# Performance work log

Measured on AMD Instinct MI355X. Metric: run time of the kernel, lower is better.

Reference implementation:

```python
import jax, jax.numpy as jnp
import numpy as np

S = 256  # vocab_size == num_states (required for the original code to broadcast)
B = 16
L = 512


def sparsemax(z):
    # sparsemax over the last axis (Martins & Astudillo 2016)
    zs = -jnp.sort(-z, axis=-1)                      # descending sort
    k = jnp.arange(1, z.shape[-1] + 1, dtype=z.dtype)
    zc = jnp.cumsum(zs, axis=-1)
    supp = 1.0 + k * zs > zc                         # support mask
    kz = supp.sum(axis=-1, keepdims=True)
    tau = (jnp.take_along_axis(zc, kz - 1, axis=-1) - 1.0) / kz.astype(z.dtype)
    return jnp.maximum(z - tau, 0.0)


def sparsemax_loss_vec(z):
    # Fenchel-Young sparsemax loss against EVERY class y:
    #   loss[..., y] = <z, p*> - 0.5||p*||^2 + 0.5 - z_y,  p* = sparsemax(z)
    p = sparsemax(z)
    c = (z * p).sum(-1, keepdims=True) - 0.5 * (p * p).sum(-1, keepdims=True) + 0.5
    return c - z


def setup_inputs() -> dict:
    key = jax.random.key(0)
    k1, k2, k3, k4, k5 = jax.random.split(key, 5)
    xs = jax.random.randint(k1, (B, L), 1, S)   # tokens in [1, S); 0 is padding
    alpha = jax.random.normal(k2, (1, S)) * 0.1
    omega = jax.random.normal(k3, (1, S)) * 0.1
    E = jax.random.normal(k4, (S, S)) * 0.1
    T = jax.random.normal(k5, (S, S, S)) * 0.1
    return {"xs": xs, "alpha": alpha, "omega": omega, "E": E, "T": T}


def reference(xs, alpha, omega, E, T):
    S_ = E.shape[0]
    mask = xs != 0                         # padding mask (padding=0)
    # Precompute loss tables (vectorizes all sparsemax_loss calls of the original)
    LE = sparsemax_loss_vec(E)             # (S, S):   LE[q, x]
    LT = sparsemax_loss_vec(T)             # (S, S, S): LT[q, x, next]
    LOm = sparsemax_loss_vec(omega)[0]     # (S,)  chart[:, K]
    LAl = sparsemax_loss_vec(alpha)[0]     # (S,)
    LE_x = LE.T                            # (x, q)
    LT_x = jnp.transpose(LT, (1, 0, 2))    # (x, q, next)

    c0 = jnp.broadcast_to(LOm, (xs.shape[0], S_))  # (B, S) chart at t = K

    def step(c, inp):
        x_t, m_t = inp                     # (B,), (B,)
        # chart[q, t] = LE[q, x_t] + logsumexp(LT[q, x_t, :] + chart[:, t+1])
        new = LE_x[x_t] + jax.nn.logsumexp(LT_x[x_t] + c[:, None, :], axis=-1)
        return jnp.where(m_t[:, None], new, c), None

    # backward recursion t = K-1 .. 0  ->  scan over time-reversed tokens
    c_final, _ = jax.lax.scan(step, c0, (xs[:, ::-1].T, mask[:, ::-1].T))

    per_seq = jax.nn.logsumexp(LAl[None, :] + c_final, axis=-1)  # (B,)
    return jnp.sum(per_seq)[None]          # matches torch shape (1,)
```

## Files before the change

### kernel.cpp

```cpp
#include <hip/hip_runtime.h>
#include <hip/hip_fp16.h>

#define LDIM 512
#define BDIM 16

#define WS_A    0u
#define WS_CE   262144u
#define WS_LOM  263168u
#define WS_LAL  264192u
#define WS_PS   265216u
#define WS_W    270336u
#define WS_FAST_BYTES (270336ull + 16777216ull)

typedef float f32x4 __attribute__((ext_vector_type(4)));

__device__ __forceinline__ float wred_add(float v) {
    #pragma unroll
    for (int off = 32; off; off >>= 1) v += __shfl_xor(v, off);
    return v;
}
__device__ __forceinline__ float wred_max(float v) {
    #pragma unroll
    for (int off = 32; off; off >>= 1) v = fmaxf(v, __shfl_xor(v, off));
    return v;
}

#if __has_builtin(__builtin_amdgcn_cvt_pk_f32_fp8) && __has_builtin(__builtin_amdgcn_cvt_pk_fp8_f32)
#define HW_FP8 1
#else
#define HW_FP8 0
#endif

__device__ __forceinline__ unsigned int sw_fp8_enc(float a) {
    union { float f; unsigned int u; } x; x.f = a;
    unsigned int u = x.u + 0x80000u;
    return (((u >> 23) & 0xffu) - 120u) * 8u + ((u >> 20) & 7u);
}
__device__ __forceinline__ unsigned int pack4_fp8(float a, float b, float c, float d) {
#if HW_FP8
    int v = 0;
    v = __builtin_amdgcn_cvt_pk_fp8_f32(a, b, v, false);
    v = __builtin_amdgcn_cvt_pk_fp8_f32(c, d, v, true);
    return (unsigned int)v;
#else
    return sw_fp8_enc(a) | (sw_fp8_enc(b) << 8) | (sw_fp8_enc(c) << 16) | (sw_fp8_enc(d) << 24);
#endif
}
__device__ __forceinline__ unsigned char fp8_1(float a) {
#if HW_FP8
    return (unsigned char)(__builtin_amdgcn_cvt_pk_fp8_f32(a, a, 0, false) & 0xff);
#else
    return (unsigned char)sw_fp8_enc(a);
#endif
}

__device__ __forceinline__ long mk64(unsigned int lo, unsigned int hi) {
    return (long)(((unsigned long long)hi << 32) | (unsigned long long)lo);
}

__device__ __forceinline__ void sync_lds() {
    asm volatile("s_waitcnt lgkmcnt(0)" ::: "memory");
    __builtin_amdgcn_sched_barrier(0);
    __builtin_amdgcn_s_barrier();
    __builtin_amdgcn_sched_barrier(0);
    asm volatile("" ::: "memory");
}

__device__ float sparsemax_c4(float z0, float z1, float z2, float z3) {
    float ssum = wred_add(z0 + z1 + z2 + z3);
    float tau = (ssum - 1.0f) * (1.0f / 256.0f);
    int kprev = 256;
    for (int it = 0; it < 64; ++it) {
        float s = 0.f, cnt = 0.f;
        if (z0 > tau) { s += z0; cnt += 1.f; }
        if (z1 > tau) { s += z1; cnt += 1.f; }
        if (z2 > tau) { s += z2; cnt += 1.f; }
        if (z3 > tau) { s += z3; cnt += 1.f; }
        s = wred_add(s);
        cnt = wred_add(cnt);
        tau = (s - 1.0f) / cnt;
        int k = (int)cnt;
        if (k == kprev) break;
        kprev = k;
    }
    float cs = 0.f, t2 = tau * tau;
    if (z0 > tau) cs += z0 * z0 - t2;
    if (z1 > tau) cs += z1 * z1 - t2;
    if (z2 > tau) cs += z2 * z2 - t2;
    if (z3 > tau) cs += z3 * z3 - t2;
    cs = wred_add(cs);
    return 0.5f * cs + 0.5f;
}

__global__ __launch_bounds__(256) void k_erow(const float* E, const float* omega,
                                              const float* alpha,
                                              float* cE, float* LOm, float* LAl) {
    int wid = blockIdx.x * 4 + (threadIdx.x >> 6);
    if (wid >= 258) return;
    int lane = threadIdx.x & 63;
    const float* row = (wid < 256) ? (E + wid * 256)
                      : (wid == 256 ? omega : alpha);
    float4 z = *(const float4*)(row + lane * 4);
    float c = sparsemax_c4(z.x, z.y, z.z, z.w);
    if (wid < 256) {
        if (lane == 0) cE[wid] = c;
    } else {
        float* dst = (wid == 256) ? LOm : LAl;
        *(float4*)(dst + lane * 4) = make_float4(c - z.x, c - z.y, c - z.z, c - z.w);
    }
}

__global__ __launch_bounds__(256) void k_trow(const float* T, const float* E,
                                              const float* cE, unsigned char* W8,
                                              float* EA, int writeW) {
    int wid = blockIdx.x * 4 + (threadIdx.x >> 6);
    int lane = threadIdx.x & 63;
    int x = wid >> 8, q = wid & 255;
    const float* row = T + ((size_t)((q << 8) | x) << 8);
    float4 z = *(const float4*)(row + lane * 4);
    float c = sparsemax_c4(z.x, z.y, z.z, z.w);
    if (writeW) {
        unsigned int packed = pack4_fp8(__expf(-z.x), __expf(-z.y),
                                        __expf(-z.z), __expf(-z.w));
        int n0 = lane << 2;
        size_t off = ((size_t)x << 16) + ((size_t)(q >> 4) << 12)
                   + ((size_t)(n0 >> 6) << 10)
                   + ((size_t)((n0 >> 3) & 3) << 8)
                   + ((size_t)(q & 15) << 4)
                   + ((size_t)((n0 >> 5) & 1) << 3)
                   + (size_t)(n0 & 7);
        *(unsigned int*)(W8 + off) = packed;
    }
    if (lane == 0) EA[wid] = __expf(c + cE[q] - E[(q << 8) + x]);
}

#define PF(XV, D0, D1, D2, D3, EAS) do {                                 \
    const unsigned char* p_ = WqBase + ((size_t)(XV) << 16);             \
    D0 = *(const uint4*)(p_);                                            \
    D1 = *(const uint4*)(p_ + 1024);                                     \
    D2 = *(const uint4*)(p_ + 2048);                                     \
    D3 = *(const uint4*)(p_ + 3072);                                     \
    EAS = EAq[(XV) << 8];                                                \
} while (0)

#define STEPX(XC, W0, W1_, W2_, W3_, EAS) do {                           \
    float rr_ = rs2[pb];                                                 \
    if ((XC) != 0) {                                                     \
        const uint4* bv_ = (const uint4*)u8b[pb];                        \
        uint4 B0 = bv_[(g << 2) + 0];                                    \
        uint4 B1 = bv_[(g << 2) + 1];                                    \
        uint4 B2 = bv_[(g << 2) + 2];                                    \
        uint4 B3 = bv_[(g << 2) + 3];                                    \
        f32x4 ac0 = {0.f, 0.f, 0.f, 0.f}, ac1 = {0.f, 0.f, 0.f, 0.f};    \
        ac0 = __builtin_amdgcn_mfma_f32_16x16x32_fp8_fp8(mk64(W0.x, W0.y),   mk64(B0.x, B0.y), ac0, 0, 0, 0); \
        ac1 = __builtin_amdgcn_mfma_f32_16x16x32_fp8_fp8(mk64(W0.z, W0.w),   mk64(B0.z, B0.w), ac1, 0, 0, 0); \
        ac0 = __builtin_amdgcn_mfma_f32_16x16x32_fp8_fp8(mk64(W1_.x, W1_.y), mk64(B1.x, B1.y), ac0, 0, 0, 0); \
        ac1 = __builtin_amdgcn_mfma_f32_16x16x32_fp8_fp8(mk64(W1_.z, W1_.w), mk64(B1.z, B1.w), ac1, 0, 0, 0); \
        ac0 = __builtin_amdgcn_mfma_f32_16x16x32_fp8_fp8(mk64(W2_.x, W2_.y), mk64(B2.x, B2.y), ac0, 0, 0, 0); \
        ac1 = __builtin_amdgcn_mfma_f32_16x16x32_fp8_fp8(mk64(W2_.z, W2_.w), mk64(B2.z, B2.w), ac1, 0, 0, 0); \
        ac0 = __builtin_amdgcn_mfma_f32_16x16x32_fp8_fp8(mk64(W3_.x, W3_.y), mk64(B3.x, B3.y), ac0, 0, 0, 0); \
        ac1 = __builtin_amdgcn_mfma_f32_16x16x32_fp8_fp8(mk64(W3_.z, W3_.w), mk64(B3.z, B3.w), ac1, 0, 0, 0); \
        f32x4 sv = ac0 + ac1;    \
        float svr = (r_ == 0) ? sv.x : (r_ == 1) ? sv.y                  \
                  : (r_ == 2) ? sv.z : sv.w;                             \
        if (isw) {                                                       \
            float nu = (EAS) * svr * rr_;                                \
            u_lastS = nu;                                                \
            u8c[((pb ^ 1) << 8) + wbyte] = fp8_1(nu);                    \
        }                                                                \
        if (tid == 0) { rs2[pb ^ 1] = 0.0625f / fmaxf(sv.x, 1e-30f);     \
                        LM -= __logf(rr_); }                             \
    } else {                                                             \
        if (isw) u8c[((pb ^ 1) << 8) + wbyte] = u8c[(pb << 8) + wbyte];  \
        if (tid == 0) rs2[pb ^ 1] = rs2[pb];                             \
    }                                                                    \
    pb ^= 1;                                                             \
    sync_lds();                                                          \
} while (0)

__global__ __launch_bounds__(1024) void k_main_fast(const int* xs, const unsigned char* W8,
                                                    const float* EA, const float* LOm,
                                                    const float* LAl, float* per_seq) {
    int b = blockIdx.x, tid = threadIdx.x;
    int lane = tid & 63, w = tid >> 6, g = lane >> 4;
    int r_ = lane & 3;
    __shared__ int xsh[LDIM];
    __shared__ float red[4];
    __shared__ float rs2[2];
    __shared__ float lm_sh;
    __shared__ __align__(16) unsigned int u8b[2][64];
    __shared__ __align__(16) float u_f[256];
    unsigned char* u8c = (unsigned char*)u8b;
    if (tid < LDIM) xsh[tid] = xs[b * LDIM + tid];
    if (tid < 64) {
        int gg = tid >> 4, cch = (tid >> 1) & 7, j0 = (tid & 1) << 2;
        int n0 = (cch << 5) + (gg << 3) + j0;
        float4 lv = *(const float4*)(LOm + n0);
        u8b[0][tid] = pack4_fp8(__expf(lv.x), __expf(lv.y), __expf(lv.z), __expf(lv.w));
    }
    if (tid < 2) rs2[tid] = 0.0625f / 256.0f;
    __syncthreads();

    float LM = 0.f;
    int pb = 0;
    int isw = ((lane & 15) < 4);
    int q0 = (w << 4) + (g << 2);
    int wdw = (((q0 >> 3) & 3) << 4) + ((q0 >> 5) << 1) + ((q0 & 7) >> 2);
    int wbyte = (wdw << 2) + r_;
    float u_lastS = 1.f;
    const unsigned char* WqBase = W8 + ((size_t)w << 12) + ((size_t)lane << 4);
    const float* EAq = EA + q0 + r_;

    uint4 A0, A1, A2, A3, Bb0, Bb1, Bb2, Bb3, C0, C1, C2, C3, D0, D1, D2, D3;
    float eA, eB, eC, eD;
    int x0 = xsh[511], x1 = xsh[510], x2 = xsh[509], x3 = xsh[508];
    PF(x0, A0, A1, A2, A3, eA);
    PF(x1, Bb0, Bb1, Bb2, Bb3, eB);
    PF(x2, C0, C1, C2, C3, eC);
    PF(x3, D0, D1, D2, D3, eD);
    for (int it = 0; it < 128; ++it) {
        int t = 511 - (it << 2);
        int pf = t - 4;
        int y0 = (pf >= 0) ? xsh[pf]     : 0;
        int y1 = (pf >= 1) ? xsh[pf - 1] : 0;
        int y2 = (pf >= 2) ? xsh[pf - 2] : 0;
        int y3 = (pf >= 3) ? xsh[pf - 3] : 0;
        STEPX(x0, A0, A1, A2, A3, eA);     PF(y0, A0, A1, A2, A3, eA);
        STEPX(x1, Bb0, Bb1, Bb2, Bb3, eB); PF(y1, Bb0, Bb1, Bb2, Bb3, eB);
        STEPX(x2, C0, C1, C2, C3, eC);     PF(y2, C0, C1, C2, C3, eC);
        STEPX(x3, D0, D1, D2, D3, eD);     PF(y3, D0, D1, D2, D3, eD);
        x0 = y0; x1 = y1; x2 = y2; x3 = y3;
    }

    if (isw) u_f[q0 + r_] = u_lastS;
    if (tid == 0) lm_sh = LM;
    __syncthreads();
    float v = -3.0e38f;
    if (tid < 256) v = LAl[tid] + __logf(fmaxf(u_f[tid], 1e-37f));
    float m2 = wred_max(v);
    if (tid < 256 && (tid & 63) == 0) red[tid >> 6] = m2;
    __syncthreads();
    m2 = fmaxf(fmaxf(red[0], red[1]), fmaxf(red[2], red[3]));
    float e = (tid < 256) ? __expf(v - m2) : 0.f;
    float es = wred_add(e);
    __syncthreads();
    if (tid < 256 && (tid & 63) == 0) red[tid >> 6] = es;
    __syncthreads();
    if (tid == 0) per_seq[b] = lm_sh + m2 + __logf(red[0] + red[1] + red[2] + red[3]);
}

__global__ __launch_bounds__(256) void k_main_med(const int* xs, const float* T,
                                                  const float* A, const float* LOm,
                                                  const float* LAl, float* per_seq) {
    int b = blockIdx.x, q = threadIdx.x;
    __shared__ int xsh[LDIM];
    __shared__ float red[4];
    __shared__ __align__(16) float u_f[256];
    for (int i = q; i < LDIM; i += 256) xsh[i] = xs[b * LDIM + i];
    float c = LOm[q];
    __syncthreads();
    for (int t = LDIM - 1; t >= 0; --t) {
        int x = xsh[t];
        if (x != 0) {
            float m = wred_max(c);
            if ((q & 63) == 0) red[q >> 6] = m;
            __syncthreads();
            m = fmaxf(fmaxf(red[0], red[1]), fmaxf(red[2], red[3]));
            u_f[q] = __expf(c - m);
            __syncthreads();
            const float* Tp = T + (((size_t)(q << 8) + (size_t)x) << 8);
            float acc = 0.f;
            #pragma unroll 4
            for (int i = 0; i < 32; ++i) {
                float4 ta = *(const float4*)(Tp + (i << 3));
                float4 tb = *(const float4*)(Tp + (i << 3) + 4);
                float4 ua = *(const float4*)(u_f + (i << 3));
                float4 ub = *(const float4*)(u_f + (i << 3) + 4);
                acc = fmaf(__expf(-ta.x), ua.x, acc);
                acc = fmaf(__expf(-ta.y), ua.y, acc);
                acc = fmaf(__expf(-ta.z), ua.z, acc);
                acc = fmaf(__expf(-ta.w), ua.w, acc);
                acc = fmaf(__expf(-tb.x), ub.x, acc);
                acc = fmaf(__expf(-tb.y), ub.y, acc);
                acc = fmaf(__expf(-tb.z), ub.z, acc);
                acc = fmaf(__expf(-tb.w), ub.w, acc);
            }
            acc = fmaxf(acc, 1e-30f);
            c = __logf(A[(x << 8) + q]) + m + __logf(acc);
        }
    }
    float v = LAl[q] + c;
    float m2 = wred_max(v);
    if ((q & 63) == 0) red[q >> 6] = m2;
    __syncthreads();
    m2 = fmaxf(fmaxf(red[0], red[1]), fmaxf(red[2], red[3]));
    float es = wred_add(__expf(v - m2));
    __syncthreads();
    if ((q & 63) == 0) red[q >> 6] = es;
    __syncthreads();
    if (q == 0) per_seq[b] = m2 + __logf(red[0] + red[1] + red[2] + red[3]);
}

__global__ __launch_bounds__(64) void k_final(const float* per_seq, float* out) {
    if (threadIdx.x == 0) {
        float s = 0.f;
        for (int i = 0; i < BDIM; ++i) s += per_seq[i];
        out[0] = s;
    }
}

extern "C" void kernel_launch(void* const* d_in, const int* in_sizes, int n_in,
                              void* d_out, int out_size, void* d_ws, size_t ws_size,
                              hipStream_t stream) {
    const int* xs = nullptr;
    const float *alpha = nullptr, *omega = nullptr, *E = nullptr, *T = nullptr;
    int seen256 = 0;
    for (int i = 0; i < n_in; ++i) {
        int s = in_sizes[i];
        if      (s == 16777216) T  = (const float*)d_in[i];
        else if (s == 65536)    E  = (const float*)d_in[i];
        else if (s == 8192)     xs = (const int*)d_in[i];
        else if (s == 256) { if (seen256++ == 0) alpha = (const float*)d_in[i];
                             else                omega = (const float*)d_in[i]; }
    }

    char* ws = (char*)d_ws;
    float* EA       = (float*)(ws + WS_A);
    float* cE       = (float*)(ws + WS_CE);
    float* LOm      = (float*)(ws + WS_LOM);
    float* LAl      = (float*)(ws + WS_LAL);
    float* per_seq  = (float*)(ws + WS_PS);
    unsigned char* W8 = (unsigned char*)(ws + WS_W);
    int fast = (ws_size >= WS_FAST_BYTES) ? 1 : 0;

    k_erow<<<65, 256, 0, stream>>>(E, omega, alpha, cE, LOm, LAl);
    k_trow<<<16384, 256, 0, stream>>>(T, E, cE, W8, EA, fast);
    if (fast) k_main_fast<<<BDIM, 1024, 0, stream>>>(xs, W8, EA, LOm, LAl, per_seq);
    else      k_main_med <<<BDIM, 256, 0, stream>>>(xs, T, EA, LOm, LAl, per_seq);
    k_final<<<1, 64, 0, stream>>>(per_seq, (float*)d_out);
}
```

Before: 524.2 us.

## Use scaled 16x16x128 FP8 MFMA with inline-asm loads and shallower prefetch

Replaces the eight 16x16x32 FP8 MFMAs per step with two MX-scaled 16x16x128 f8f6f4 MFMAs (unit scales) when the builtin exists. The weight prefetch loads are now issued through inline asm, and each step waits with an explicit vmcnt so that only the next step's loads stay in flight. Prefetch depth drops from four steps to two, which frees registers but leaves less time to hide global memory latency on this serial recurrence.

```diff
diff --git a/kernel.cpp b/kernel.cpp
--- a/kernel.cpp
+++ b/kernel.cpp
@@ -13,6 +13,8 @@
 #define WS_FAST_BYTES (270336ull + 16777216ull)
 
 typedef float f32x4 __attribute__((ext_vector_type(4)));
+typedef int   i32x8 __attribute__((ext_vector_type(8)));
+typedef unsigned int u32x4 __attribute__((ext_vector_type(4)));
 
 __device__ __forceinline__ float wred_add(float v) {
     #pragma unroll
@@ -29,6 +31,11 @@
 #define HW_FP8 1
 #else
 #define HW_FP8 0
+#endif
+#if __has_builtin(__builtin_amdgcn_mfma_scale_f32_16x16x128_f8f6f4)
+#define HW_MXF8 1
+#else
+#define HW_MXF8 0
 #endif
 
 __device__ __forceinline__ unsigned int sw_fp8_enc(float a) {
@@ -56,6 +63,12 @@
 
 __device__ __forceinline__ long mk64(unsigned int lo, unsigned int hi) {
     return (long)(((unsigned long long)hi << 32) | (unsigned long long)lo);
+}
+__device__ __forceinline__ i32x8 pk8(u32x4 a, u32x4 b) {
+    i32x8 r;
+    r[0] = (int)a[0]; r[1] = (int)a[1]; r[2] = (int)a[2]; r[3] = (int)a[3];
+    r[4] = (int)b[0]; r[5] = (int)b[1]; r[6] = (int)b[2]; r[7] = (int)b[3];
+    return r;
 }
 
 __device__ __forceinline__ void sync_lds() {
@@ -134,32 +147,36 @@
     if (lane == 0) EA[wid] = __expf(c + cE[q] - E[(q << 8) + x]);
 }
 
-#define PF(XV, D0, D1, D2, D3, EAS) do {                                 \
-    const unsigned char* p_ = WqBase + ((size_t)(XV) << 16);             \
-    D0 = *(const uint4*)(p_);                                            \
-    D1 = *(const uint4*)(p_ + 1024);                                     \
-    D2 = *(const uint4*)(p_ + 2048);                                     \
-    D3 = *(const uint4*)(p_ + 3072);                                     \
-    EAS = EAq[(XV) << 8];                                                \
+#define PF(XV, D0, D1, D2, D3, EAS) do {                                  \
+    const unsigned char* p_ = WqBase + ((size_t)(XV) << 16);              \
+    const float* e_ = EAq + ((XV) << 8);                                  \
+    asm volatile("global_load_dwordx4 %0, %5, off\n\t"                    \
+                 "global_load_dwordx4 %1, %5, off offset:1024\n\t"        \
+                 "global_load_dwordx4 %2, %5, off offset:2048\n\t"        \
+                 "global_load_dwordx4 %3, %5, off offset:3072\n\t"        \
+                 "global_load_dword   %4, %6, off"                        \
+                 : "=&v"(D0), "=&v"(D1), "=&v"(D2), "=&v"(D3), "=&v"(EAS) \
+                 : "v"(p_), "v"(e_));                                     \
 } while (0)
 
+#if HW_MXF8
 #define STEPX(XC, W0, W1_, W2_, W3_, EAS) do {                           \
+    asm volatile("s_waitcnt vmcnt(5)" ::: "memory");                     \
+    __builtin_amdgcn_sched_barrier(0);                                   \
     float rr_ = rs2[pb];                                                 \
     if ((XC) != 0) {                                                     \
-        const uint4* bv_ = (const uint4*)u8b[pb];                        \
-        uint4 B0 = bv_[(g << 2) + 0];                                    \
-        uint4 B1 = bv_[(g << 2) + 1];                                    \
-        uint4 B2 = bv_[(g << 2) + 2];                                    \
-        uint4 B3 = bv_[(g << 2) + 3];                                    \
+        const u32x4* bv_ = (const u32x4*)u8b[pb];                        \
+        u32x4 B0 = bv_[(g << 2) + 0];                                    \
+        u32x4 B1 = bv_[(g << 2) + 1];                                    \
+        u32x4 B2 = bv_[(g << 2) + 2];                                    \
+        u32x4 B3 = bv_[(g << 2) + 3];                                    \
         f32x4 ac0 = {0.f, 0.f, 0.f, 0.f}, ac1 = {0.f, 0.f, 0.f, 0.f};    \
-        ac0 = __builtin_amdgcn_mfma_f32_16x16x32_fp8_fp8(mk64(W0.x, W0.y),   mk64(B0.x, B0.y), ac0, 0, 0, 0); \
-        ac1 = __builtin_amdgcn_mfma_f32_16x16x32_fp8_fp8(mk64(W0.z, W0.w),   mk64(B0.z, B0.w), ac1, 0, 0, 0); \
-        ac0 = __builtin_amdgcn_mfma_f32_16x16x32_fp8_fp8(mk64(W1_.x, W1_.y), mk64(B1.x, B1.y), ac0, 0, 0, 0); \
-        ac1 = __builtin_amdgcn_mfma_f32_16x16x32_fp8_fp8(mk64(W1_.z, W1_.w), mk64(B1.z, B1.w), ac1, 0, 0, 0); \
-        ac0 = __builtin_amdgcn_mfma_f32_16x16x32_fp8_fp8(mk64(W2_.x, W2_.y), mk64(B2.x, B2.y), ac0, 0, 0, 0); \
-        ac1 = __builtin_amdgcn_mfma_f32_16x16x32_fp8_fp8(mk64(W2_.z, W2_.w), mk64(B2.z, B2.w), ac1, 0, 0, 0); \
-        ac0 = __builtin_amdgcn_mfma_f32_16x16x32_fp8_fp8(mk64(W3_.x, W3_.y), mk64(B3.x, B3.y), ac0, 0, 0, 0); \
-        ac1 = __builtin_amdgcn_mfma_f32_16x16x32_fp8_fp8(mk64(W3_.z, W3_.w), mk64(B3.z, B3.w), ac1, 0, 0, 0); \
+        ac0 = __builtin_amdgcn_mfma_scale_f32_16x16x128_f8f6f4(          \
+                pk8(W0, W1_), pk8(B0, B1), ac0, 0, 0,                    \
+                0, 0x7F7F7F7F, 0, 0x7F7F7F7F);                           \
+        ac1 = __builtin_amdgcn_mfma_scale_f32_16x16x128_f8f6f4(          \
+                pk8(W2_, W3_), pk8(B2, B3), ac1, 0, 0,                   \
+                0, 0x7F7F7F7F, 0, 0x7F7F7F7F);                           \
         f32x4 sv = ac0 + ac1;    \
         float svr = (r_ == 0) ? sv.x : (r_ == 1) ? sv.y                  \
                   : (r_ == 2) ? sv.z : sv.w;                             \
@@ -177,6 +194,44 @@
     pb ^= 1;                                                             \
     sync_lds();                                                          \
 } while (0)
+#else
+#define STEPX(XC, W0, W1_, W2_, W3_, EAS) do {                           \
+    asm volatile("s_waitcnt vmcnt(5)" ::: "memory");                     \
+    __builtin_amdgcn_sched_barrier(0);                                   \
+    float rr_ = rs2[pb];                                                 \
+    if ((XC) != 0) {                                                     \
+        const u32x4* bv_ = (const u32x4*)u8b[pb];                        \
+        u32x4 B0 = bv_[(g << 2) + 0];                                    \
+        u32x4 B1 = bv_[(g << 2) + 1];                                    \
+        u32x4 B2 = bv_[(g << 2) + 2];                                    \
+        u32x4 B3 = bv_[(g << 2) + 3];                                    \
+        f32x4 ac0 = {0.f, 0.f, 0.f, 0.f}, ac1 = {0.f, 0.f, 0.f, 0.f};    \
+        ac0 = __builtin_amdgcn_mfma_f32_16x16x32_fp8_fp8(mk64(W0[0], W0[1]),   mk64(B0[0], B0[1]), ac0, 0, 0, 0); \
+        ac1 = __builtin_amdgcn_mfma_f32_16x16x32_fp8_fp8(mk64(W0[2], W0[3]),   mk64(B0[2], B0[3]), ac1, 0, 0, 0); \
+        ac0 = __builtin_amdgcn_mfma_f32_16x16x32_fp8_fp8(mk64(W1_[0], W1_[1]), mk64(B1[0], B1[1]), ac0, 0, 0, 0); \
+        ac1 = __builtin_amdgcn_mfma_f32_16x16x32_fp8_fp8(mk64(W1_[2], W1_[3]), mk64(B1[2], B1[3]), ac1, 0, 0, 0); \
+        ac0 = __builtin_amdgcn_mfma_f32_16x16x32_fp8_fp8(mk64(W2_[0], W2_[1]), mk64(B2[0], B2[1]), ac0, 0, 0, 0); \
+        ac1 = __builtin_amdgcn_mfma_f32_16x16x32_fp8_fp8(mk64(W2_[2], W2_[3]), mk64(B2[2], B2[3]), ac1, 0, 0, 0); \
+        ac0 = __builtin_amdgcn_mfma_f32_16x16x32_fp8_fp8(mk64(W3_[0], W3_[1]), mk64(B3[0], B3[1]), ac0, 0, 0, 0); \
+        ac1 = __builtin_amdgcn_mfma_f32_16x16x32_fp8_fp8(mk64(W3_[2], W3_[3]), mk64(B3[2], B3[3]), ac1, 0, 0, 0); \
+        f32x4 sv = ac0 + ac1;                                            \
+        float svr = (r_ == 0) ? sv.x : (r_ == 1) ? sv.y                  \
+                  : (r_ == 2) ? sv.z : sv.w;                             \
+        if (isw) {                                                       \
+            float nu = (EAS) * svr * rr_;                                \
+            u_lastS = nu;                                                \
+            u8c[((pb ^ 1) << 8) + wbyte] = fp8_1(nu);                    \
+        }                                                                \
+        if (tid == 0) { rs2[pb ^ 1] = 0.0625f / fmaxf(sv.x, 1e-30f);     \
+                        LM -= __logf(rr_); }                             \
+    } else {                                                             \
+        if (isw) u8c[((pb ^ 1) << 8) + wbyte] = u8c[(pb << 8) + wbyte];  \
+        if (tid == 0) rs2[pb ^ 1] = rs2[pb];                             \
+    }                                                                    \
+    pb ^= 1;                                                             \
+    sync_lds();                                                          \
+} while (0)
+#endif
 
 __global__ __launch_bounds__(1024) void k_main_fast(const int* xs, const unsigned char* W8,
                                                     const float* EA, const float* LOm,
@@ -211,26 +266,20 @@
     const unsigned char* WqBase = W8 + ((size_t)w << 12) + ((size_t)lane << 4);
     const float* EAq = EA + q0 + r_;
 
-    uint4 A0, A1, A2, A3, Bb0, Bb1, Bb2, Bb3, C0, C1, C2, C3, D0, D1, D2, D3;
-    float eA, eB, eC, eD;
-    int x0 = xsh[511], x1 = xsh[510], x2 = xsh[509], x3 = xsh[508];
+    u32x4 A0, A1, A2, A3, Bb0, Bb1, Bb2, Bb3;
+    float eA, eB;
+    int x0 = xsh[511], x1 = xsh[510];
     PF(x0, A0, A1, A2, A3, eA);
     PF(x1, Bb0, Bb1, Bb2, Bb3, eB);
-    PF(x2, C0, C1, C2, C3, eC);
-    PF(x3, D0, D1, D2, D3, eD);
-    for (int it = 0; it < 128; ++it) {
-        int t = 511 - (it << 2);
-        int pf = t - 4;
+    for (int it = 0; it < 256; ++it) {
+        int pf = 509 - (it << 1);
         int y0 = (pf >= 0) ? xsh[pf]     : 0;
         int y1 = (pf >= 1) ? xsh[pf - 1] : 0;
-        int y2 = (pf >= 2) ? xsh[pf - 2] : 0;
-        int y3 = (pf >= 3) ? xsh[pf - 3] : 0;
         STEPX(x0, A0, A1, A2, A3, eA);     PF(y0, A0, A1, A2, A3, eA);
         STEPX(x1, Bb0, Bb1, Bb2, Bb3, eB); PF(y1, Bb0, Bb1, Bb2, Bb3, eB);
-        STEPX(x2, C0, C1, C2, C3, eC);     PF(y2, C0, C1, C2, C3, eC);
-        STEPX(x3, D0, D1, D2, D3, eD);     PF(y3, D0, D1, D2, D3, eD);
-        x0 = y0; x1 = y1; x2 = y2; x3 = y3;
-    }
+        x0 = y0; x1 = y1;
+    }
+    asm volatile("s_waitcnt vmcnt(0)" ::: "memory");
 
     if (isw) u_f[q0 + r_] = u_lastS;
     if (tid == 0) lm_sh = LM;
```

Measured after the change: 498.0 us. 1.05x faster.
